# Kernel tuning notes

Measured on AMD Instinct MI355X. Metric: run time of the kernel, lower is better.

Reference implementation:

```python
import jax, jax.numpy as jnp
import numpy as np

B, T, N, H = 1024, 256, 32, 64  # batch, SEQ_LEN, N_SERIES, RNN_HID_SIZE
EPS = 1e-05


def setup_inputs() -> dict:
    key = jax.random.key(0)
    ks = jax.random.split(key, 24)
    s_h = 1.0 / np.sqrt(H)
    s_n = 1.0 / np.sqrt(N)
    u = lambda k, shape, s: jax.random.uniform(k, shape, jnp.float32, -s, s)
    inp = {
        'values': jax.random.normal(ks[0], (B, T, N), jnp.float32),
        'masks': (jax.random.uniform(ks[1], (B, T, N)) < 0.8).astype(jnp.float32),
        'deltas': jax.random.uniform(ks[2], (B, T, N), jnp.float32) * 5.0,
        'evals': jax.random.normal(ks[3], (B, T, N), jnp.float32),
        'eval_masks': (jax.random.uniform(ks[4], (B, T, N)) < 0.1).astype(jnp.float32),
        'labels': (jax.random.uniform(ks[5], (B, 1)) < 0.5).astype(jnp.float32),
        'is_train': jnp.ones((B, 1), jnp.float32),
        # TemporalDecay h: Linear(N->H)
        'td_h_W': u(ks[6], (H, N), s_h), 'td_h_b': u(ks[7], (H,), s_h),
        # TemporalDecay x: diag Linear(N->N)
        'td_x_W': u(ks[8], (N, N), s_n), 'td_x_b': u(ks[9], (N,), s_n),
        # hist_reg: Linear(H->N)
        'hist_W': u(ks[10], (N, H), s_n), 'hist_b': u(ks[11], (N,), s_n),
        # feat_reg: masked Linear(N->N), mask = 1 - I
        'feat_W': u(ks[12], (N, N), s_n), 'feat_b': u(ks[13], (N,), s_n),
        # weight_combine: Linear(2N->N)
        'wc_W': u(ks[14], (N, 2 * N), s_n), 'wc_b': u(ks[15], (N,), s_n),
        # LSTMCell(2N -> H)
        'W_ih': u(ks[16], (4 * H, 2 * N), s_h), 'W_hh': u(ks[17], (4 * H, H), s_h),
        'b_ih': u(ks[18], (4 * H,), s_h), 'b_hh': u(ks[19], (4 * H,), s_h),
        # out: Linear(H->1)
        'out_W': u(ks[20], (1, H), s_h), 'out_b': u(ks[21], (1,), s_h),
    }
    return inp


def _rits_forward(values, masks, deltas, labels, is_train,
                  td_h_W, td_h_b, td_x_W, td_x_b, hist_W, hist_b,
                  feat_W, feat_b, wc_W, wc_b, W_ih, W_hh, b_ih, b_hh,
                  out_W, out_b):
    # time-major for scan: [T, B, N]
    vals_t = jnp.swapaxes(values, 0, 1)
    masks_t = jnp.swapaxes(masks, 0, 1)
    delts_t = jnp.swapaxes(deltas, 0, 1)

    feat_mask = 1.0 - jnp.eye(N, dtype=values.dtype)
    td_x_diag = jnp.diagonal(td_x_W)                  # W * eye(N) linear == elementwise diag

    def step(carry, xmd):
        h, c, x_loss = carry
        x, m, d = xmd
        gamma_h = jnp.exp(-jax.nn.relu(d @ td_h_W.T + td_h_b))   # [B,H]
        gamma_x = jnp.exp(-jax.nn.relu(d * td_x_diag + td_x_b))  # [B,N]
        h = h * gamma_h
        x_h = h @ hist_W.T + hist_b
        msum = jnp.sum(m) + EPS
        x_loss = x_loss + jnp.sum(jnp.abs(x - x_h) * m) / msum
        x_c = m * x + (1.0 - m) * x_h
        z_h = x_c @ (feat_W * feat_mask).T + feat_b
        x_loss = x_loss + jnp.sum(jnp.abs(x - z_h) * m) / msum
        alpha = jnp.concatenate([gamma_x, m], axis=1) @ wc_W.T + wc_b
        c_h = alpha * z_h + (1.0 - alpha) * x_h
        x_loss = x_loss + jnp.sum(jnp.abs(x - c_h) * m) / msum
        c_c = m * x + (1.0 - m) * c_h
        inputs = jnp.concatenate([c_c, m], axis=1)  # [B, 2N]
        gates = inputs @ W_ih.T + b_ih + h @ W_hh.T + b_hh
        i, f, g, o = jnp.split(gates, 4, axis=1)
        c = jax.nn.sigmoid(f) * c + jax.nn.sigmoid(i) * jnp.tanh(g)
        h = jax.nn.sigmoid(o) * jnp.tanh(c)
        return (h, c, x_loss), c_c

    h0 = jnp.zeros((values.shape[0], H), values.dtype)
    c0 = jnp.zeros((values.shape[0], H), values.dtype)
    (h, c, x_loss), imps = jax.lax.scan(step, (h0, c0, jnp.float32(0.0)),
                                        (vals_t, masks_t, delts_t))
    imputations = jnp.swapaxes(imps, 0, 1)  # [B, T, N]

    y_h = h @ out_W.T + out_b  # logits [B,1]
    # binary_cross_entropy_with_logits, reduce=False
    max_val = jnp.maximum(-y_h, 0.0)
    bce = y_h - y_h * labels + max_val + jnp.log(jnp.exp(-max_val) + jnp.exp(-y_h - max_val))
    y_loss = jnp.sum(bce * is_train) / (jnp.sum(is_train) + EPS)
    loss = x_loss / T + y_loss * 0.1
    predictions = jax.nn.sigmoid(y_h)
    return loss, predictions, imputations


def reference(values, masks, deltas, evals, eval_masks, labels, is_train,
              td_h_W, td_h_b, td_x_W, td_x_b, hist_W, hist_b, feat_W, feat_b,
              wc_W, wc_b, W_ih, W_hh, b_ih, b_hh, out_W, out_b):
    loss, predictions, imputations = _rits_forward(
        values, masks, deltas, labels, is_train,
        td_h_W, td_h_b, td_x_W, td_x_b, hist_W, hist_b,
        feat_W, feat_b, wc_W, wc_b, W_ih, W_hh, b_ih, b_hh, out_W, out_b)
    return loss, predictions, imputations
```

## Files before the change

### kernel.cpp

```cpp
#include <hip/hip_runtime.h>

#define EPSF 1e-5f

typedef _Float16 h2f  __attribute__((ext_vector_type(2)));
typedef _Float16 h8   __attribute__((ext_vector_type(8)));
typedef float    f32x4 __attribute__((ext_vector_type(4)));

#if defined(__has_builtin)
#if __has_builtin(__builtin_amdgcn_fdot2)
#define HAVE_FDOT2 1
#endif
#endif

__device__ __forceinline__ float fsig(float x){ return 1.0f/(1.0f+__expf(-x)); }
__device__ __forceinline__ float ftanh(float x){
  float e = __expf(2.f*x);
  float r = (e-1.f)/(e+1.f);
  return (x > 15.f) ? 1.f : ((x < -15.f) ? -1.f : r);
}
__device__ __forceinline__ int pkf(float lo, float hi){
  return __builtin_bit_cast(int, __builtin_amdgcn_cvt_pkrtz(lo, hi));
}
__device__ __forceinline__ int4 mk4(const float* p){
  return make_int4(pkf(p[0],p[1]),pkf(p[2],p[3]),pkf(p[4],p[5]),pkf(p[6],p[7]));
}
__device__ __forceinline__ float dot2(int w, int x, float acc){
#ifdef HAVE_FDOT2
  return __builtin_amdgcn_fdot2(__builtin_bit_cast(h2f, w),
                                __builtin_bit_cast(h2f, x), acc, false);
#else
  h2f a = __builtin_bit_cast(h2f, w), b = __builtin_bit_cast(h2f, x);
  return acc + (float)a[0]*(float)b[0] + (float)a[1]*(float)b[1];
#endif
}
__device__ __forceinline__ int rl_i(int v, int l){ return __builtin_amdgcn_readlane(v, l); }
__device__ __forceinline__ float rl_f(float v, int l){
  return __int_as_float(__builtin_amdgcn_readlane(__float_as_int(v), l));
}
#define BAR() do{ asm volatile("s_waitcnt lgkmcnt(0)" ::: "memory"); __builtin_amdgcn_s_barrier(); }while(0)

__global__ void msum_kernel(const float* __restrict__ masks, float* __restrict__ msum){
  const int t   = blockIdx.x;
  const int tid = threadIdx.x;
  const int b0  = tid >> 3;
  const int n4  = (tid & 7) << 2;
  float s = 0.f;
  #pragma unroll 4
  for (int i = 0; i < 32; ++i) {
    const int b = b0 + (i << 5);
    const float4 v = *reinterpret_cast<const float4*>(masks + ((size_t)b*256 + t)*32 + n4);
    s += v.x + v.y + v.z + v.w;
  }
  __shared__ float red[256];
  red[tid] = s; __syncthreads();
  for (int off = 128; off > 0; off >>= 1) {
    if (tid < off) red[tid] += red[tid + off];
    __syncthreads();
  }
  if (tid == 0) msum[t] = red[0] + EPSF;
}

__global__ __launch_bounds__(512, 1) void rits_kernel(
  const float* __restrict__ values, const float* __restrict__ masks,
  const float* __restrict__ deltas, const float* __restrict__ labels,
  const float* __restrict__ is_train,
  const float* __restrict__ td_h_W, const float* __restrict__ td_h_b,
  const float* __restrict__ td_x_W, const float* __restrict__ td_x_b,
  const float* __restrict__ hist_W, const float* __restrict__ hist_b,
  const float* __restrict__ feat_W, const float* __restrict__ feat_b,
  const float* __restrict__ wc_W,  const float* __restrict__ wc_b,
  const float* __restrict__ W_ih,  const float* __restrict__ W_hh,
  const float* __restrict__ b_ih,  const float* __restrict__ b_hh,
  const float* __restrict__ out_W, const float* __restrict__ out_b,
  const float* __restrict__ msum,
  float* __restrict__ xl_acc, float* __restrict__ bce_acc,
  float* __restrict__ predictions, float* __restrict__ imps)
{
  __shared__ __align__(16) int  inp_s[4][84];
  __shared__ float gp[4][256];
  __shared__ float msum_l[256];

  const int tid = threadIdx.x;
  const int b   = blockIdx.x;
  const int wv  = tid >> 6;
  const int ln  = tid & 63;
  const bool chain = (wv < 4);
  const int me  = wv & 3;
  const int b2  = (b << 2) | me;

  if (tid < 256) msum_l[tid] = 1.0f / msum[tid];

  int4 Wb[2][4];
  const int kg = ln >> 4;
  #pragma unroll
  for (int nt = 0; nt < 2; ++nt){
    const int col = (wv << 5) + (nt << 4) + (ln & 15);
    #pragma unroll
    for (int ks = 0; ks < 4; ++ks){
      const int k0 = (ks << 5) + (kg << 3);
      const float* src = (k0 < 64) ? (W_ih + (size_t)col*64 + k0)
                                   : (W_hh + (size_t)col*64 + (k0 - 64));
      Wb[nt][ks] = make_int4(pkf(src[0],src[1]), pkf(src[2],src[3]),
                             pkf(src[4],src[5]), pkf(src[6],src[7]));
    }
  }
  const int col0 = (wv << 5) + (ln & 15);
  const float bs0 = b_ih[col0]      + b_hh[col0];
  const float bs1 = b_ih[col0 + 16] + b_hh[col0 + 16];

  int4  fB[4];
  int4  fC[8];
  int4  fDa[8];
  float wz[32];
  float thb_r=0.f, tdxd_r=0.f, tdxb_r=0.f, histb_r=0.f, featb_r=0.f, wcb_r=0.f;
  float xv=0.f, mv=0.f, dv=0.f;
  if (chain){
    const int nr = ln & 31;
    #pragma unroll
    for (int g = 0; g < 4; ++g) fB[g] = mk4(td_h_W + ln*32 + 8*g);
    #pragma unroll
    for (int g = 0; g < 8; ++g) fC[g] = mk4(hist_W + nr*64 + 8*g);
    #pragma unroll
    for (int g = 0; g < 8; ++g) fDa[g] = mk4(wc_W + nr*64 + 8*g);
    #pragma unroll
    for (int k = 0; k < 32; ++k) wz[k] = (k==nr) ? 0.f : feat_W[nr*32 + k];
    thb_r = td_h_b[ln];
    if (ln < 32){
      tdxd_r  = td_x_W[ln*33];
      tdxb_r  = td_x_b[ln];
      histb_r = hist_b[ln];
      featb_r = feat_b[ln];
      wcb_r   = wc_b[ln];
      const size_t base = (size_t)b2*8192 + ln;
      xv = values[base]; mv = masks[base]; dv = deltas[base];
    }
  }
  float h_reg = 0.f, c_reg = 0.f, loss_acc = 0.f;

  __syncthreads();

  for (int t = 0; t < 256; ++t){
    if (chain){
      const float x_cur = xv, m_cur = mv, d_cur = dv;
      float gx_r = 0.f;
      if (ln < 32){
        gx_r = __expf(-fmaxf(fmaf(d_cur, tdxd_r, tdxb_r), 0.f));
        if (t < 255){
          const size_t base = (size_t)b2*8192 + (size_t)(t+1)*32 + ln;
          xv = values[base]; mv = masks[base]; dv = deltas[base];
        }
      }
      const int i0 = (2*ln) & 63, i1 = (2*ln+1) & 63;
      const int dw = pkf(__shfl(d_cur, i0), __shfl(d_cur, i1));
      const int j0 = (2*ln-32) & 63, j1 = (2*ln-31) & 63;
      const float ga  = __shfl(gx_r,  i0), gb  = __shfl(gx_r,  i1);
      const float ma_ = __shfl(m_cur, j0), mb_ = __shfl(m_cur, j1);
      const int aw = (ln < 16) ? pkf(ga, gb) : pkf(ma_, mb_);

      {
        float a0 = thb_r, a1 = 0.f;
        #pragma unroll
        for (int g4 = 0; g4 < 4; ++g4){
          const int4 w = fB[g4];
          a0 = dot2(w.x, rl_i(dw, 4*g4+0), a0);
          a1 = dot2(w.y, rl_i(dw, 4*g4+1), a1);
          a0 = dot2(w.z, rl_i(dw, 4*g4+2), a0);
          a1 = dot2(w.w, rl_i(dw, 4*g4+3), a1);
        }
        h_reg *= __expf(-fmaxf(a0+a1, 0.f));
      }
      const int hw = pkf(__shfl(h_reg, i0), __shfl(h_reg, i1));
      float xh_v = 0.f, x_c_v = 0.f;
      if (ln < 32){
        float a0 = histb_r, a1 = 0.f, a2 = 0.f, a3 = 0.f;
        #pragma unroll
        for (int g4 = 0; g4 < 8; ++g4){
          const int4 w = fC[g4];
          a0 = dot2(w.x, rl_i(hw, 4*g4+0), a0);
          a1 = dot2(w.y, rl_i(hw, 4*g4+1), a1);
          a2 = dot2(w.z, rl_i(hw, 4*g4+2), a2);
          a3 = dot2(w.w, rl_i(hw, 4*g4+3), a3);
        }
        xh_v  = (a0+a1)+(a2+a3);
        x_c_v = m_cur*x_cur + (1.f-m_cur)*xh_v;
      }
      float ccv = 0.f;
      if (ln < 32){
        float z0 = featb_r, z1 = 0.f, z2 = 0.f, z3 = 0.f;
        #pragma unroll
        for (int k = 0; k < 32; k += 4){
          z0 = fmaf(rl_f(x_c_v, k+0), wz[k+0], z0);
          z1 = fmaf(rl_f(x_c_v, k+1), wz[k+1], z1);
          z2 = fmaf(rl_f(x_c_v, k+2), wz[k+2], z2);
          z3 = fmaf(rl_f(x_c_v, k+3), wz[k+3], z3);
        }
        const float z = (z0+z1)+(z2+z3);
        float a0 = wcb_r, a1 = 0.f, a2 = 0.f, a3 = 0.f;
        #pragma unroll
        for (int g4 = 0; g4 < 8; ++g4){
          const int4 w = fDa[g4];
          a0 = dot2(w.x, rl_i(aw, 4*g4+0), a0);
          a1 = dot2(w.y, rl_i(aw, 4*g4+1), a1);
          a2 = dot2(w.z, rl_i(aw, 4*g4+2), a2);
          a3 = dot2(w.w, rl_i(aw, 4*g4+3), a3);
        }
        const float al = (a0+a1)+(a2+a3);
        const float ch = al*z + (1.f-al)*xh_v;
        loss_acc += (fabsf(x_cur-xh_v)+fabsf(x_cur-z)+fabsf(x_cur-ch))*m_cur*msum_l[t];
        ccv = m_cur*x_cur + (1.f-m_cur)*ch;
        imps[(size_t)b2*8192 + (size_t)t*32 + ln] = ccv;
      }
      const int ccw = pkf(__shfl(ccv, i0), __shfl(ccv, i1));
      inp_s[me][ln] = (ln < 16) ? ccw : (ln < 32 ? aw : hw);
    }

    BAR();

    {
      const int arow = ln & 15;
      int4 A[4];
      if (arow < 4){
        #pragma unroll
        for (int ks = 0; ks < 4; ++ks)
          A[ks] = *reinterpret_cast<const int4*>(&inp_s[arow][(ks << 4) + (kg << 2)]);
      } else {
        #pragma unroll
        for (int ks = 0; ks < 4; ++ks) A[ks] = make_int4(0,0,0,0);
      }
      f32x4 acc0 = {bs0, bs0, bs0, bs0};
      f32x4 acc1 = {bs1, bs1, bs1, bs1};
      #pragma unroll
      for (int ks = 0; ks < 4; ++ks){
        acc0 = __builtin_amdgcn_mfma_f32_16x16x32_f16(
                 __builtin_bit_cast(h8, A[ks]), __builtin_bit_cast(h8, Wb[0][ks]), acc0, 0,0,0);
        acc1 = __builtin_amdgcn_mfma_f32_16x16x32_f16(
                 __builtin_bit_cast(h8, A[ks]), __builtin_bit_cast(h8, Wb[1][ks]), acc1, 0,0,0);
      }
      if (kg == 0){
        #pragma unroll
        for (int e = 0; e < 4; ++e){
          gp[e][col0]      = acc0[e];
          gp[e][col0 + 16] = acc1[e];
        }
      }
    }

    BAR();

    if (chain){
      const float ig = gp[me][ln];
      const float fg = gp[me][64+ln];
      const float gg = gp[me][128+ln];
      const float og = gp[me][192+ln];
      c_reg = fsig(fg)*c_reg + fsig(ig)*ftanh(gg);
      h_reg = fsig(og)*ftanh(c_reg);
    }
  }

  if (chain){
    float l = loss_acc;
    l += __shfl_xor(l,16); l += __shfl_xor(l,8);
    l += __shfl_xor(l,4);  l += __shfl_xor(l,2); l += __shfl_xor(l,1);
    if (ln == 0) atomicAdd(xl_acc, l);

    float p = h_reg * out_W[ln];
    p += __shfl_xor(p,32); p += __shfl_xor(p,16); p += __shfl_xor(p,8);
    p += __shfl_xor(p,4);  p += __shfl_xor(p,2);  p += __shfl_xor(p,1);
    if (ln == 0){
      const float y = p + out_b[0];
      predictions[b2] = fsig(y);
      const float lab = labels[b2];
      const float it  = is_train[b2];
      const float mx  = fmaxf(-y, 0.f);
      const float bce = y - y*lab + mx + __logf(__expf(-mx) + __expf(-y - mx));
      atomicAdd(bce_acc, bce * it);
    }
  }
}

__global__ void final_kernel(const float* __restrict__ is_train,
                             const float* __restrict__ ws,
                             float* __restrict__ out){
  const int tid = threadIdx.x;
  __shared__ float red[256];
  red[tid] = is_train[tid] + is_train[tid+256] + is_train[tid+512] + is_train[tid+768];
  __syncthreads();
  for (int off = 128; off > 0; off >>= 1){
    if (tid < off) red[tid] += red[tid + off];
    __syncthreads();
  }
  if (tid == 0){
    const float yl = ws[1] / (red[0] + EPSF);
    out[0] = ws[0] / 256.0f + 0.1f * yl;
  }
}

extern "C" void kernel_launch(void* const* d_in, const int* in_sizes, int n_in,
                              void* d_out, int out_size, void* d_ws, size_t ws_size,
                              hipStream_t stream){
  const float* values   = (const float*)d_in[0];
  const float* masks    = (const float*)d_in[1];
  const float* deltas   = (const float*)d_in[2];
  const float* labels   = (const float*)d_in[5];
  const float* is_train = (const float*)d_in[6];
  const float* td_h_W   = (const float*)d_in[7];
  const float* td_h_b   = (const float*)d_in[8];
  const float* td_x_W   = (const float*)d_in[9];
  const float* td_x_b   = (const float*)d_in[10];
  const float* hist_W   = (const float*)d_in[11];
  const float* hist_b   = (const float*)d_in[12];
  const float* feat_W   = (const float*)d_in[13];
  const float* feat_b   = (const float*)d_in[14];
  const float* wc_W     = (const float*)d_in[15];
  const float* wc_b     = (const float*)d_in[16];
  const float* W_ih     = (const float*)d_in[17];
  const float* W_hh     = (const float*)d_in[18];
  const float* b_ih     = (const float*)d_in[19];
  const float* b_hh     = (const float*)d_in[20];
  const float* out_W    = (const float*)d_in[21];
  const float* out_b    = (const float*)d_in[22];

  float* out = (float*)d_out;
  float* ws  = (float*)d_ws;

  hipMemsetAsync(ws, 0, 2*sizeof(float), stream);
  msum_kernel<<<256, 256, 0, stream>>>(masks, ws + 2);
  rits_kernel<<<256, 512, 0, stream>>>(values, masks, deltas, labels, is_train,
      td_h_W, td_h_b, td_x_W, td_x_b, hist_W, hist_b, feat_W, feat_b,
      wc_W, wc_b, W_ih, W_hh, b_ih, b_hh, out_W, out_b,
      ws + 2, ws + 0, ws + 1, out + 1, out + 1 + 1024);
  final_kernel<<<1, 256, 0, stream>>>(is_train, ws, out);
}
```

Before: 458.2 us.

## Pack two outputs per lane and move per-step weights to shared memory

Each chain lane now computes two adjacent hidden/feature outputs and keeps its values in packed half-pairs. This removes the cross-lane shuffles that previously built packed operands each step. The small recurrent weights (temporal decay, history, feature regression, weight combine) move from per-lane registers to packed half tables in shared memory. The feature regression also switches from fp32 FMAs to fdot2. Register pressure and shuffles go down, at the cost of LDS reads every timestep, half the lanes idling in each stage, and some extra fp16 rounding in the feature regression.

```diff
diff --git a/kernel.cpp b/kernel.cpp
--- a/kernel.cpp
+++ b/kernel.cpp
@@ -34,9 +34,6 @@
 #endif
 }
 __device__ __forceinline__ int rl_i(int v, int l){ return __builtin_amdgcn_readlane(v, l); }
-__device__ __forceinline__ float rl_f(float v, int l){
-  return __int_as_float(__builtin_amdgcn_readlane(__float_as_int(v), l));
-}
 #define BAR() do{ asm volatile("s_waitcnt lgkmcnt(0)" ::: "memory"); __builtin_amdgcn_s_barrier(); }while(0)
 
 __global__ void msum_kernel(const float* __restrict__ masks, float* __restrict__ msum){
@@ -76,6 +73,10 @@
   float* __restrict__ xl_acc, float* __restrict__ bce_acc,
   float* __restrict__ predictions, float* __restrict__ imps)
 {
+  __shared__ __align__(16) int4 pkB[8][32];
+  __shared__ __align__(16) int4 pkC[16][16];
+  __shared__ __align__(16) int4 pkZ[8][16];
+  __shared__ __align__(16) int4 pkDa[16][16];
   __shared__ __align__(16) int  inp_s[4][84];
   __shared__ float gp[4][256];
   __shared__ float msum_l[256];
@@ -89,6 +90,18 @@
   const int b2  = (b << 2) | me;
 
   if (tid < 256) msum_l[tid] = 1.0f / msum[tid];
+  if (tid < 256){ const int l = tid & 31, g = (tid >> 5) & 3, r = tid >> 7;
+    pkB[r*4+g][l] = mk4(td_h_W + (2*l+r)*32 + 8*g); }
+  if (tid < 256){ const int l = tid & 15, g = (tid >> 4) & 7, r = tid >> 7;
+    pkC[r*8+g][l] = mk4(hist_W + (2*l+r)*64 + 8*g); }
+  if (tid < 128){ const int l = tid & 15, g = (tid >> 4) & 3, r = tid >> 6;
+    const int row = 2*l + r, c0 = 8*g;
+    float v[8];
+    #pragma unroll
+    for (int k = 0; k < 8; ++k){ const int c = c0+k; v[k] = (c==row) ? 0.f : feat_W[row*32+c]; }
+    pkZ[r*4+g][l] = make_int4(pkf(v[0],v[1]),pkf(v[2],v[3]),pkf(v[4],v[5]),pkf(v[6],v[7])); }
+  if (tid < 256){ const int l = tid & 15, g = (tid >> 4) & 7, r = tid >> 7;
+    pkDa[r*8+g][l] = mk4(wc_W + (2*l+r)*64 + 8*g); }
 
   int4 Wb[2][4];
   const int kg = ln >> 4;
@@ -108,110 +121,123 @@
   const float bs0 = b_ih[col0]      + b_hh[col0];
   const float bs1 = b_ih[col0 + 16] + b_hh[col0 + 16];
 
-  int4  fB[4];
-  int4  fC[8];
-  int4  fDa[8];
-  float wz[32];
-  float thb_r=0.f, tdxd_r=0.f, tdxb_r=0.f, histb_r=0.f, featb_r=0.f, wcb_r=0.f;
-  float xv=0.f, mv=0.f, dv=0.f;
+  float2 thb = {0.f,0.f}, histb = {0.f,0.f}, featb = {0.f,0.f}, wcb = {0.f,0.f};
+  float2 tdxb = {0.f,0.f}, ow = {0.f,0.f};
+  float tdxd0 = 0.f, tdxd1 = 0.f;
+  float x0=0.f,x1=0.f, m0=0.f,m1=0.f, d0=0.f,d1=0.f;
+  float h0=0.f,h1=0.f, c0=0.f,c1=0.f;
+  float loss_acc = 0.f;
   if (chain){
-    const int nr = ln & 31;
-    #pragma unroll
-    for (int g = 0; g < 4; ++g) fB[g] = mk4(td_h_W + ln*32 + 8*g);
-    #pragma unroll
-    for (int g = 0; g < 8; ++g) fC[g] = mk4(hist_W + nr*64 + 8*g);
-    #pragma unroll
-    for (int g = 0; g < 8; ++g) fDa[g] = mk4(wc_W + nr*64 + 8*g);
-    #pragma unroll
-    for (int k = 0; k < 32; ++k) wz[k] = (k==nr) ? 0.f : feat_W[nr*32 + k];
-    thb_r = td_h_b[ln];
     if (ln < 32){
-      tdxd_r  = td_x_W[ln*33];
-      tdxb_r  = td_x_b[ln];
-      histb_r = hist_b[ln];
-      featb_r = feat_b[ln];
-      wcb_r   = wc_b[ln];
-      const size_t base = (size_t)b2*8192 + ln;
-      xv = values[base]; mv = masks[base]; dv = deltas[base];
-    }
-  }
-  float h_reg = 0.f, c_reg = 0.f, loss_acc = 0.f;
+      thb = *(const float2*)(td_h_b + 2*ln);
+      ow  = *(const float2*)(out_W + 2*ln);
+    }
+    if (ln < 16){
+      histb = *(const float2*)(hist_b + 2*ln);
+      featb = *(const float2*)(feat_b + 2*ln);
+      wcb   = *(const float2*)(wc_b   + 2*ln);
+      tdxb  = *(const float2*)(td_x_b + 2*ln);
+      tdxd0 = td_x_W[(2*ln)*33]; tdxd1 = td_x_W[(2*ln+1)*33];
+      const size_t base = (size_t)b2*8192 + 2*ln;
+      const float2 xv = *(const float2*)(values + base);
+      const float2 mv = *(const float2*)(masks  + base);
+      const float2 dv = *(const float2*)(deltas + base);
+      x0=xv.x; x1=xv.y; m0=mv.x; m1=mv.y; d0=dv.x; d1=dv.y;
+    }
+  }
 
   __syncthreads();
 
   for (int t = 0; t < 256; ++t){
     if (chain){
-      const float x_cur = xv, m_cur = mv, d_cur = dv;
-      float gx_r = 0.f;
+      const float xc0_=x0, xc1_=x1, mc0=m0, mc1=m1, dc0=d0, dc1=d1;
+      int dw=0, mw=0, gxw=0;
+      if (ln < 16){
+        dw = pkf(dc0, dc1);
+        mw = pkf(mc0, mc1);
+        const float g0 = __expf(-fmaxf(fmaf(dc0, tdxd0, tdxb.x), 0.f));
+        const float g1 = __expf(-fmaxf(fmaf(dc1, tdxd1, tdxb.y), 0.f));
+        gxw = pkf(g0, g1);
+        if (t < 255){
+          const size_t base = (size_t)b2*8192 + (size_t)(t+1)*32 + 2*ln;
+          const float2 xv = *(const float2*)(values + base);
+          const float2 mv = *(const float2*)(masks  + base);
+          const float2 dv = *(const float2*)(deltas + base);
+          x0=xv.x; x1=xv.y; m0=mv.x; m1=mv.y; d0=dv.x; d1=dv.y;
+        }
+      }
+      int hw = 0;
       if (ln < 32){
-        gx_r = __expf(-fmaxf(fmaf(d_cur, tdxd_r, tdxb_r), 0.f));
-        if (t < 255){
-          const size_t base = (size_t)b2*8192 + (size_t)(t+1)*32 + ln;
-          xv = values[base]; mv = masks[base]; dv = deltas[base];
-        }
-      }
-      const int i0 = (2*ln) & 63, i1 = (2*ln+1) & 63;
-      const int dw = pkf(__shfl(d_cur, i0), __shfl(d_cur, i1));
-      const int j0 = (2*ln-32) & 63, j1 = (2*ln-31) & 63;
-      const float ga  = __shfl(gx_r,  i0), gb  = __shfl(gx_r,  i1);
-      const float ma_ = __shfl(m_cur, j0), mb_ = __shfl(m_cur, j1);
-      const int aw = (ln < 16) ? pkf(ga, gb) : pkf(ma_, mb_);
-
-      {
-        float a0 = thb_r, a1 = 0.f;
-        #pragma unroll
-        for (int g4 = 0; g4 < 4; ++g4){
-          const int4 w = fB[g4];
-          a0 = dot2(w.x, rl_i(dw, 4*g4+0), a0);
-          a1 = dot2(w.y, rl_i(dw, 4*g4+1), a1);
-          a0 = dot2(w.z, rl_i(dw, 4*g4+2), a0);
-          a1 = dot2(w.w, rl_i(dw, 4*g4+3), a1);
-        }
-        h_reg *= __expf(-fmaxf(a0+a1, 0.f));
-      }
-      const int hw = pkf(__shfl(h_reg, i0), __shfl(h_reg, i1));
-      float xh_v = 0.f, x_c_v = 0.f;
-      if (ln < 32){
-        float a0 = histb_r, a1 = 0.f, a2 = 0.f, a3 = 0.f;
-        #pragma unroll
-        for (int g4 = 0; g4 < 8; ++g4){
-          const int4 w = fC[g4];
-          a0 = dot2(w.x, rl_i(hw, 4*g4+0), a0);
-          a1 = dot2(w.y, rl_i(hw, 4*g4+1), a1);
-          a2 = dot2(w.z, rl_i(hw, 4*g4+2), a2);
-          a3 = dot2(w.w, rl_i(hw, 4*g4+3), a3);
-        }
-        xh_v  = (a0+a1)+(a2+a3);
-        x_c_v = m_cur*x_cur + (1.f-m_cur)*xh_v;
-      }
-      float ccv = 0.f;
-      if (ln < 32){
-        float z0 = featb_r, z1 = 0.f, z2 = 0.f, z3 = 0.f;
-        #pragma unroll
-        for (int k = 0; k < 32; k += 4){
-          z0 = fmaf(rl_f(x_c_v, k+0), wz[k+0], z0);
-          z1 = fmaf(rl_f(x_c_v, k+1), wz[k+1], z1);
-          z2 = fmaf(rl_f(x_c_v, k+2), wz[k+2], z2);
-          z3 = fmaf(rl_f(x_c_v, k+3), wz[k+3], z3);
-        }
-        const float z = (z0+z1)+(z2+z3);
-        float a0 = wcb_r, a1 = 0.f, a2 = 0.f, a3 = 0.f;
-        #pragma unroll
-        for (int g4 = 0; g4 < 8; ++g4){
-          const int4 w = fDa[g4];
-          a0 = dot2(w.x, rl_i(aw, 4*g4+0), a0);
-          a1 = dot2(w.y, rl_i(aw, 4*g4+1), a1);
-          a2 = dot2(w.z, rl_i(aw, 4*g4+2), a2);
-          a3 = dot2(w.w, rl_i(aw, 4*g4+3), a3);
-        }
-        const float al = (a0+a1)+(a2+a3);
-        const float ch = al*z + (1.f-al)*xh_v;
-        loss_acc += (fabsf(x_cur-xh_v)+fabsf(x_cur-z)+fabsf(x_cur-ch))*m_cur*msum_l[t];
-        ccv = m_cur*x_cur + (1.f-m_cur)*ch;
-        imps[(size_t)b2*8192 + (size_t)t*32 + ln] = ccv;
-      }
-      const int ccw = pkf(__shfl(ccv, i0), __shfl(ccv, i1));
-      inp_s[me][ln] = (ln < 16) ? ccw : (ln < 32 ? aw : hw);
+        float a00=thb.x, a01=0.f, a10=thb.y, a11=0.f;
+        #pragma unroll
+        for (int g = 0; g < 4; ++g){
+          const int4 w0 = pkB[g][ln];
+          const int4 w1 = pkB[4+g][ln];
+          a00 = dot2(w0.x, rl_i(dw,4*g+0), a00); a01 = dot2(w0.y, rl_i(dw,4*g+1), a01);
+          a00 = dot2(w0.z, rl_i(dw,4*g+2), a00); a01 = dot2(w0.w, rl_i(dw,4*g+3), a01);
+          a10 = dot2(w1.x, rl_i(dw,4*g+0), a10); a11 = dot2(w1.y, rl_i(dw,4*g+1), a11);
+          a10 = dot2(w1.z, rl_i(dw,4*g+2), a10); a11 = dot2(w1.w, rl_i(dw,4*g+3), a11);
+        }
+        h0 *= __expf(-fmaxf(a00+a01, 0.f));
+        h1 *= __expf(-fmaxf(a10+a11, 0.f));
+        hw = pkf(h0, h1);
+        inp_s[me][32+ln] = hw;
+      }
+      float ccw_v = 0.f;
+      if (ln < 16){
+        float b00=histb.x, b01=0.f, b10=histb.y, b11=0.f;
+        #pragma unroll
+        for (int g = 0; g < 8; ++g){
+          const int4 w0 = pkC[g][ln];
+          const int4 w1 = pkC[8+g][ln];
+          b00 = dot2(w0.x, rl_i(hw,4*g+0), b00); b01 = dot2(w0.y, rl_i(hw,4*g+1), b01);
+          b00 = dot2(w0.z, rl_i(hw,4*g+2), b00); b01 = dot2(w0.w, rl_i(hw,4*g+3), b01);
+          b10 = dot2(w1.x, rl_i(hw,4*g+0), b10); b11 = dot2(w1.y, rl_i(hw,4*g+1), b11);
+          b10 = dot2(w1.z, rl_i(hw,4*g+2), b10); b11 = dot2(w1.w, rl_i(hw,4*g+3), b11);
+        }
+        const float xh0 = b00+b01, xh1 = b10+b11;
+        const float q0 = mc0*xc0_ + (1.f-mc0)*xh0;
+        const float q1 = mc1*xc1_ + (1.f-mc1)*xh1;
+        const int xcw = pkf(q0, q1);
+        float z00=featb.x, z01=0.f, z10=featb.y, z11=0.f;
+        #pragma unroll
+        for (int g = 0; g < 4; ++g){
+          const int4 w0 = pkZ[g][ln];
+          const int4 w1 = pkZ[4+g][ln];
+          z00 = dot2(w0.x, rl_i(xcw,4*g+0), z00); z01 = dot2(w0.y, rl_i(xcw,4*g+1), z01);
+          z00 = dot2(w0.z, rl_i(xcw,4*g+2), z00); z01 = dot2(w0.w, rl_i(xcw,4*g+3), z01);
+          z10 = dot2(w1.x, rl_i(xcw,4*g+0), z10); z11 = dot2(w1.y, rl_i(xcw,4*g+1), z11);
+          z10 = dot2(w1.z, rl_i(xcw,4*g+2), z10); z11 = dot2(w1.w, rl_i(xcw,4*g+3), z11);
+        }
+        const float z0v = z00+z01, z1v = z10+z11;
+        float a00=wcb.x, a01=0.f, a10=wcb.y, a11=0.f;
+        #pragma unroll
+        for (int g = 0; g < 8; ++g){
+          const int4 w0 = pkDa[g][ln];
+          const int4 w1 = pkDa[8+g][ln];
+          const int k0 = 4*g;
+          const int s0 = (k0   < 16) ? rl_i(gxw,k0  ) : rl_i(mw,k0-16);
+          const int s1 = (k0+1 < 16) ? rl_i(gxw,k0+1) : rl_i(mw,k0-15);
+          const int s2 = (k0+2 < 16) ? rl_i(gxw,k0+2) : rl_i(mw,k0-14);
+          const int s3 = (k0+3 < 16) ? rl_i(gxw,k0+3) : rl_i(mw,k0-13);
+          a00 = dot2(w0.x, s0, a00); a01 = dot2(w0.y, s1, a01);
+          a00 = dot2(w0.z, s2, a00); a01 = dot2(w0.w, s3, a01);
+          a10 = dot2(w1.x, s0, a10); a11 = dot2(w1.y, s1, a11);
+          a10 = dot2(w1.z, s2, a10); a11 = dot2(w1.w, s3, a11);
+        }
+        const float al0 = a00+a01, al1 = a10+a11;
+        const float ch0 = al0*z0v + (1.f-al0)*xh0;
+        const float ch1 = al1*z1v + (1.f-al1)*xh1;
+        loss_acc += ((fabsf(xc0_-xh0)+fabsf(xc0_-z0v)+fabsf(xc0_-ch0))*mc0
+                   + (fabsf(xc1_-xh1)+fabsf(xc1_-z1v)+fabsf(xc1_-ch1))*mc1) * msum_l[t];
+        const float cc0 = mc0*xc0_ + (1.f-mc0)*ch0;
+        const float cc1 = mc1*xc1_ + (1.f-mc1)*ch1;
+        *(float2*)(imps + (size_t)b2*8192 + (size_t)t*32 + 2*ln) = make_float2(cc0,cc1);
+        ccw_v = 0.f;
+        inp_s[me][ln]      = pkf(cc0, cc1);
+        inp_s[me][16+ln]   = mw;
+      }
+      (void)ccw_v;
     }
 
     BAR();
@@ -247,23 +273,25 @@
 
     BAR();
 
-    if (chain){
-      const float ig = gp[me][ln];
-      const float fg = gp[me][64+ln];
-      const float gg = gp[me][128+ln];
-      const float og = gp[me][192+ln];
-      c_reg = fsig(fg)*c_reg + fsig(ig)*ftanh(gg);
-      h_reg = fsig(og)*ftanh(c_reg);
+    if (chain && ln < 32){
+      const float2 gi = *(const float2*)&gp[me][2*ln];
+      const float2 gf = *(const float2*)&gp[me][64+2*ln];
+      const float2 gg = *(const float2*)&gp[me][128+2*ln];
+      const float2 go = *(const float2*)&gp[me][192+2*ln];
+      c0 = fsig(gf.x)*c0 + fsig(gi.x)*ftanh(gg.x);
+      c1 = fsig(gf.y)*c1 + fsig(gi.y)*ftanh(gg.y);
+      h0 = fsig(go.x)*ftanh(c0);
+      h1 = fsig(go.y)*ftanh(c1);
     }
   }
 
   if (chain){
-    float l = loss_acc;
-    l += __shfl_xor(l,16); l += __shfl_xor(l,8);
-    l += __shfl_xor(l,4);  l += __shfl_xor(l,2); l += __shfl_xor(l,1);
+    float l = (ln < 16) ? loss_acc : 0.f;
+    l += __shfl_xor(l,32); l += __shfl_xor(l,16); l += __shfl_xor(l,8);
+    l += __shfl_xor(l,4);  l += __shfl_xor(l,2);  l += __shfl_xor(l,1);
     if (ln == 0) atomicAdd(xl_acc, l);
 
-    float p = h_reg * out_W[ln];
+    float p = (ln < 32) ? (h0*ow.x + h1*ow.y) : 0.f;
     p += __shfl_xor(p,32); p += __shfl_xor(p,16); p += __shfl_xor(p,8);
     p += __shfl_xor(p,4);  p += __shfl_xor(p,2);  p += __shfl_xor(p,1);
     if (ln == 0){
```

After: 516.3 us. 12.7% more time.
